# Kernel tuning notes

Hardware: AMD Instinct MI355X
Metric: run time of the kernel (lower is better)

## Reference

```python
import jax, jax.numpy as jnp
import numpy as np

B, T, C, H = 1, 1024, 2048, 32
N = C // H  # head_dim = 64
EPS_GN = 0.00064


def setup_inputs() -> dict:
    key = jax.random.key(0)
    ks = jax.random.split(key, 40)
    f32 = jnp.float32

    def rn(k, shape, s):
        return jax.random.normal(k, shape, f32) * s

    layer_idx, n_layer = 12, 24
    r01 = layer_idx / (n_layer - 1)
    r1a0 = 1.0 - layer_idx / n_layer
    ddd = (jnp.arange(C, dtype=f32) / C).reshape(1, 1, C)
    decay_speed = -7.0 + 5.0 * (jnp.arange(C, dtype=f32) / (C - 1)) ** (0.85 + r01 ** 0.5)

    inp = dict(
        hidden_states=jax.random.normal(ks[0], (B, T, C), f32),
        Wq=rn(ks[1], (C, C), 0.02), Wk=rn(ks[2], (C, C), 0.02),
        Wv=rn(ks[3], (C, C), 0.02), Wo=rn(ks[4], (C, C), 0.02),
        time_maa_x=1.0 - ddd ** (0.6 * r1a0 ** 0.9),
        time_maa_rg=rn(ks[5], (1, 1, C), 0.01),
        time_maa_wa=rn(ks[6], (1, 1, C), 0.01),
        time_maa_k=rn(ks[7], (1, 1, C), 0.01),
        time_maa_v=rn(ks[8], (1, 1, C), 0.01),
        time_maa_w1=rn(ks[9], (C, 4 * 32), 0.01),
        time_maa_w2=rn(ks[10], (4, 32, C), 0.01),
        time_decay=decay_speed.reshape(1, 1, C) + 0.5,
        time_decay_w1=rn(ks[11], (C, 64), 0.01),
        time_decay_w2=rn(ks[12], (64, C), 0.01),
        time_aaaaa=rn(ks[13], (1, 1, C), 0.01),
        time_aaa_w1=rn(ks[14], (C, 16), 0.01),
        time_aaa_w2=rn(ks[15], (16, C), 0.01),
        time_kkk_w1=rn(ks[16], (C, 16), 0.01),
        time_kkk_w2=rn(ks[17], (16, C), 0.01),
        gate_w1=rn(ks[18], (C, 128), 0.01),
        gate_w2=rn(ks[19], (128, C), 0.01),
        time_misc_a=rn(ks[20], (1, 1, C), 0.01),
        ma_w1=rn(ks[21], (C, 16), 0.01),
        ma_w2=rn(ks[22], (16, C), 0.01),
        time_misc_k=rn(ks[23], (1, 1, C), 0.01),
        mk_w1=rn(ks[24], (C, 16), 0.01),
        mk_w2=rn(ks[25], (16, C), 0.01),
        time_faaaa=rn(ks[26], (1, 1, H, N), 0.01),
        ln_w=1.0 + rn(ks[27], (C,), 0.01),
        ln_b=rn(ks[28], (C,), 0.01),
    )
    return inp


def _wkv7(r, w, k, v, a, b):
    """RWKV7 matrix-state recurrence. Inputs [B,T,C]; per head state [N,N].
    state_t = state * exp(w_t) (per key-col) + (state @ a_t) b_t^T + v_t k_t^T;
    out_t = state_t @ r_t."""
    hs = lambda x: x.reshape(B, T, H, N)
    r, k, v, a, b = map(hs, (r, k, v, a, b))
    dec = jnp.exp(hs(w))  # w <= -0.5, decay in (0,1)

    def step(state, inp):
        r_t, d_t, k_t, v_t, a_t, b_t = inp  # each [B,H,N]
        sa = jnp.einsum('bhij,bhj->bhi', state, a_t)
        state = (state * d_t[:, :, None, :]
                 + sa[..., None] * b_t[:, :, None, :]
                 + v_t[..., None] * k_t[:, :, None, :])
        out = jnp.einsum('bhij,bhj->bhi', state, r_t)
        return state, out

    xs = tuple(jnp.moveaxis(t, 1, 0) for t in (r, dec, k, v, a, b))  # [T,B,H,N]
    state0 = jnp.zeros((B, H, N, N), r.dtype)
    _, out = jax.lax.scan(step, state0, xs)
    return jnp.moveaxis(out, 0, 1).reshape(B, T, C)


def _group_norm(x, w, b):
    xg = x.reshape(B, T, H, N)
    mu = xg.mean(-1, keepdims=True)
    var = xg.var(-1, keepdims=True)
    xn = (xg - mu) * jax.lax.rsqrt(var + EPS_GN)
    return xn.reshape(B, T, C) * w + b


def reference(hidden_states, Wq, Wk, Wv, Wo, time_maa_x, time_maa_rg, time_maa_wa,
              time_maa_k, time_maa_v, time_maa_w1, time_maa_w2, time_decay,
              time_decay_w1, time_decay_w2, time_aaaaa, time_aaa_w1, time_aaa_w2,
              time_kkk_w1, time_kkk_w2, gate_w1, gate_w2, time_misc_a, ma_w1, ma_w2,
              time_misc_k, mk_w1, mk_w2, time_faaaa, ln_w, ln_b):
    x = hidden_states  # T already multiple of 16, so no padding branch
    dxprev = jnp.pad(x, ((0, 0), (1, 0), (0, 0)))[:, :-1] - x  # token shift
    xxx = x + dxprev * time_maa_x
    mix = jnp.tanh(xxx @ time_maa_w1).reshape(B, T, 4, 32)
    mix = jnp.einsum('btfd,fdc->fbtc', mix, time_maa_w2)  # [4,B,T,C]
    mrg, mwa, mk_mix, mv = mix[0], mix[1], mix[2], mix[3]
    xrg = x + dxprev * (time_maa_rg + mrg)
    xwa = x + dxprev * (time_maa_wa + mwa)
    xk = x + dxprev * (time_maa_k + mk_mix)
    xv = x + dxprev * (time_maa_v + mv)

    r = xrg @ Wq
    w = -jax.nn.softplus(-(time_decay + jnp.tanh(xwa @ time_decay_w1) @ time_decay_w2)) - 0.5
    k = xk @ Wk
    v = xv @ Wv
    g = jnp.tanh(xrg @ gate_w1) @ gate_w2

    kk = k + jnp.tanh(xk @ time_kkk_w1) @ time_kkk_w2
    kkh = kk.reshape(B, T, H, N)
    kk = (kkh / jnp.maximum(jnp.linalg.norm(kkh, axis=-1, keepdims=True), 1e-12)).reshape(B, T, C)

    a = jax.nn.sigmoid(time_aaaaa + (xwa @ time_aaa_w1) @ time_aaa_w2)
    ma = jax.nn.sigmoid(time_misc_a + (xwa @ ma_w1) @ ma_w2)
    k = k * ma + k * a * (1.0 - ma)
    mk_g = jax.nn.sigmoid(time_misc_k + (xk @ mk_w1) @ mk_w2)
    k = k * jnp.exp(jnp.minimum(w * mk_g, 0.0))

    y = _wkv7(r, w, k, v, -kk, kk * a)
    y = _group_norm(y, ln_w, ln_b)
    rh, kh, vh = (t.reshape(B, T, H, N) for t in (r, k, v))
    y = y + ((rh * kh * time_faaaa).sum(-1, keepdims=True) * vh).reshape(B, T, C)
    return (y * g) @ Wo
```

## Files before the change

kernel.cpp:

```cpp
#include <hip/hip_runtime.h>


#define T_ 1024
#define C_ 2048
#define H_ 32
#define N_ 64

using half8  = __attribute__((ext_vector_type(8))) _Float16;
using half4  = __attribute__((ext_vector_type(4))) _Float16;
using floatx4 = __attribute__((ext_vector_type(4))) float;

#define DPP_ADD(v, ctrl) \
    ((v) + __int_as_float(__builtin_amdgcn_update_dpp( \
        0, __float_as_int(v), (ctrl), 0xf, 0xf, true)))
#define REDUCE16(v) do { \
    v = DPP_ADD(v, 0xB1); v = DPP_ADD(v, 0x4E); \
    v = DPP_ADD(v, 0x141); v = DPP_ADD(v, 0x140); } while (0)

__device__ __forceinline__ void async_cp16(const void* g, void* l) {
    __builtin_amdgcn_global_load_lds(
        (const __attribute__((address_space(1))) void*)g,
        (__attribute__((address_space(3))) void*)l, 16, 0, 0);
}

__global__ __launch_bounds__(256) void k_tr(
    const float* __restrict__ W0, const float* __restrict__ W1,
    const float* __restrict__ W2, const float* __restrict__ W3,
    _Float16* __restrict__ D0, _Float16* __restrict__ D1,
    _Float16* __restrict__ D2, _Float16* __restrict__ D3)
{
    const int z = blockIdx.z;
    const float* S = (z == 0) ? W0 : (z == 1) ? W1 : (z == 2) ? W2 : W3;
    _Float16* D = (z == 0) ? D0 : (z == 1) ? D1 : (z == 2) ? D2 : D3;
    const int nb = blockIdx.x * 64, kb = blockIdx.y * 64;
    __shared__ __align__(16) float tile[64][65];
    const int tr = threadIdx.x >> 4, tc4 = (threadIdx.x & 15) * 4;
#pragma unroll
    for (int p = 0; p < 4; ++p) {
        int row = p * 16 + tr;
        float4 v = *(const float4*)&S[(size_t)(kb + row) * C_ + nb + tc4];
        tile[row][tc4 + 0] = v.x; tile[row][tc4 + 1] = v.y;
        tile[row][tc4 + 2] = v.z; tile[row][tc4 + 3] = v.w;
    }
    __syncthreads();
#pragma unroll
    for (int p = 0; p < 4; ++p) {
        int n = p * 16 + tr;
        half4 u;
        u[0] = (_Float16)tile[tc4 + 0][n];
        u[1] = (_Float16)tile[tc4 + 1][n];
        u[2] = (_Float16)tile[tc4 + 2][n];
        u[3] = (_Float16)tile[tc4 + 3][n];
        *(half4*)&D[(size_t)(nb + n) * C_ + kb + tc4] = u;
    }
}

__global__ __launch_bounds__(256) void k_trW(
    const float* __restrict__ maa_w1, const float* __restrict__ gate_w1,
    const float* __restrict__ decay_w1, const float* __restrict__ aaa_w1,
    const float* __restrict__ ma_w1, const float* __restrict__ kkk_w1,
    const float* __restrict__ mk_w1,
    _Float16* __restrict__ WTm, _Float16* __restrict__ WTl)
{
    const int z = blockIdx.z;
    const int k = blockIdx.x * 256 + threadIdx.x;
    const int n = blockIdx.y;
    if (z == 0 && n >= 128) return;
    const float* src; int stride, col;
    _Float16* dst;
    if (z == 0) { src = maa_w1; stride = 128; col = n; dst = WTm; }
    else {
        dst = WTl;
        if (n < 128)      { src = gate_w1;  stride = 128; col = n; }
        else if (n < 192) { src = decay_w1; stride = 64;  col = n - 128; }
        else if (n < 208) { src = aaa_w1;   stride = 16;  col = n - 192; }
        else if (n < 224) { src = ma_w1;    stride = 16;  col = n - 208; }
        else if (n < 240) { src = kkk_w1;   stride = 16;  col = n - 224; }
        else              { src = mk_w1;    stride = 16;  col = n - 240; }
    }
    dst[(size_t)n * C_ + k] = (_Float16)src[(size_t)k * stride + col];
}

__global__ __launch_bounds__(256) void k_prep(
    const float* __restrict__ X, const float* __restrict__ maa_x,
    _Float16* __restrict__ xxxH)
{
    const size_t idx = (size_t)blockIdx.x * 256 + threadIdx.x;
    const int c = (int)(idx & (C_ - 1));
    float cur = X[idx];
    float prev = (idx >= C_) ? X[idx - C_] : 0.0f;
    xxxH[idx] = (_Float16)(cur + (prev - cur) * maa_x[c]);
}

__global__ __launch_bounds__(256) void k_lora(
    int which,
    const _Float16* __restrict__ Axxx, const _Float16* __restrict__ Axrg,
    const _Float16* __restrict__ Axwa, const _Float16* __restrict__ Axk,
    const _Float16* __restrict__ WTm, const _Float16* __restrict__ WTl,
    float* __restrict__ m1p, float* __restrict__ l2p)
{
    const int mt = blockIdx.x;
    const int nt = blockIdx.y;
    const int ks = blockIdx.z;
    const _Float16* A; const _Float16* BT; float* O; int ostride;
    if (which == 0) { A = Axxx; BT = WTm; O = m1p; ostride = 128; }
    else {
        BT = WTl; O = l2p; ostride = 256;
        A = (nt < 4) ? Axrg : (nt < 7) ? Axwa : Axk;
    }
    O += (size_t)ks * T_ * ostride;
    const int m0 = mt * 64, n0 = nt * 32, k0 = ks * 512;
    const int tid = threadIdx.x;
    __shared__ __align__(16) _Float16 As[64 * 40];
    __shared__ __align__(16) _Float16 Bs[32 * 40];
    const int lane = tid & 63, wv = tid >> 6;
    const int r16 = lane & 15, q = lane >> 4;

    floatx4 acc[2];
    { floatx4 zv = {0.f, 0.f, 0.f, 0.f}; acc[0] = zv; acc[1] = zv; }

    const int arow = tid >> 2, ac8 = (tid & 3) * 8;
    const _Float16* ag = A + (size_t)(m0 + arow) * C_ + k0 + ac8;
    const _Float16* bg = BT + (size_t)(n0 + (tid >> 2)) * C_ + k0 + ac8;

    for (int kc = 0; kc < 512; kc += 32) {
        half8 av = *(const half8*)(ag + kc);
        half8 bv;
        if (tid < 128) bv = *(const half8*)(bg + kc);
        *(half8*)&As[arow * 40 + ac8] = av;
        if (tid < 128) *(half8*)&Bs[(tid >> 2) * 40 + ac8] = bv;
        __syncthreads();
        half8 af = *(const half8*)&As[(wv * 16 + r16) * 40 + q * 8];
        half8 b0 = *(const half8*)&Bs[(r16) * 40 + q * 8];
        half8 b1 = *(const half8*)&Bs[(16 + r16) * 40 + q * 8];
        acc[0] = __builtin_amdgcn_mfma_f32_16x16x32_f16(af, b0, acc[0], 0, 0, 0);
        acc[1] = __builtin_amdgcn_mfma_f32_16x16x32_f16(af, b1, acc[1], 0, 0, 0);
        __syncthreads();
    }
#pragma unroll
    for (int j = 0; j < 2; ++j)
#pragma unroll
        for (int e = 0; e < 4; ++e) {
            int row = m0 + wv * 16 + q * 4 + e;
            int col = n0 + j * 16 + r16;
            O[(size_t)row * ostride + col] = acc[j][e];
        }
}

__global__ __launch_bounds__(256) void k_xmix(
    const float* __restrict__ X, const float* __restrict__ m1p,
    const float* __restrict__ w2,
    const float* __restrict__ mrg, const float* __restrict__ mwa,
    const float* __restrict__ mk, const float* __restrict__ mv,
    _Float16* __restrict__ xrgH, _Float16* __restrict__ xwaH,
    _Float16* __restrict__ xkH, _Float16* __restrict__ xvH)
{
    const int tid = threadIdx.x;
    const int c = blockIdx.x * 256 + tid;
    const int t0 = blockIdx.y * 16;
    const size_t P = (size_t)T_ * 128;
    __shared__ __align__(16) float m1s[16][128];
#pragma unroll
    for (int p = 0; p < 2; ++p) {
        int id = tid + p * 256;
        int r = id >> 5, c4 = (id & 31) * 4;
        size_t off = (size_t)(t0 + r) * 128 + c4;
        float4 v0 = *(const float4*)&m1p[off];
        float4 v1 = *(const float4*)&m1p[P + off];
        float4 v2 = *(const float4*)&m1p[2 * P + off];
        float4 v3 = *(const float4*)&m1p[3 * P + off];
        float4 v;
        v.x = tanhf(((v0.x + v1.x) + v2.x) + v3.x);
        v.y = tanhf(((v0.y + v1.y) + v2.y) + v3.y);
        v.z = tanhf(((v0.z + v1.z) + v2.z) + v3.z);
        v.w = tanhf(((v0.w + v1.w) + v2.w) + v3.w);
        *(float4*)&m1s[r][c4] = v;
    }
    __syncthreads();
    float a0[16], a1[16], a2[16], a3[16];
#pragma unroll
    for (int t = 0; t < 16; ++t) { a0[t] = 0.f; a1[t] = 0.f; a2[t] = 0.f; a3[t] = 0.f; }
    for (int d = 0; d < 32; ++d) {
        float w0 = w2[(size_t)(0 * 32 + d) * C_ + c];
        float w1 = w2[(size_t)(1 * 32 + d) * C_ + c];
        float w2v = w2[(size_t)(2 * 32 + d) * C_ + c];
        float w3 = w2[(size_t)(3 * 32 + d) * C_ + c];
#pragma unroll
        for (int t = 0; t < 16; ++t) {
            a0[t] = fmaf(m1s[t][d],      w0,  a0[t]);
            a1[t] = fmaf(m1s[t][32 + d], w1,  a1[t]);
            a2[t] = fmaf(m1s[t][64 + d], w2v, a2[t]);
            a3[t] = fmaf(m1s[t][96 + d], w3,  a3[t]);
        }
    }
    float vrg = mrg[c], vwa = mwa[c], vmk = mk[c], vmv = mv[c];
    float prev = (t0 > 0) ? X[(size_t)(t0 - 1) * C_ + c] : 0.0f;
    for (int t = 0; t < 16; ++t) {
        size_t idx = (size_t)(t0 + t) * C_ + c;
        float cur = X[idx];
        float dx = prev - cur;
        xrgH[idx] = (_Float16)(cur + dx * (vrg + a0[t]));
        xwaH[idx] = (_Float16)(cur + dx * (vwa + a1[t]));
        xkH[idx]  = (_Float16)(cur + dx * (vmk + a2[t]));
        xvH[idx]  = (_Float16)(cur + dx * (vmv + a3[t]));
        prev = cur;
    }
}

__global__ __launch_bounds__(256) void k_gemm(
    const _Float16* __restrict__ A0, const _Float16* __restrict__ B0, float* __restrict__ C0,
    const _Float16* __restrict__ A1, const _Float16* __restrict__ B1, float* __restrict__ C1,
    const _Float16* __restrict__ A2, const _Float16* __restrict__ B2, float* __restrict__ C2)
{
    const int z = blockIdx.z;
    const _Float16* A = (z == 0) ? A0 : (z == 1) ? A1 : A2;
    const _Float16* Bt = (z == 0) ? B0 : (z == 1) ? B1 : B2;
    float* C = (z == 0) ? C0 : (z == 1) ? C1 : C2;
    const int mtile = blockIdx.y * 128;
    const int ntile = blockIdx.x * 128;
    const int tid = threadIdx.x;
    __shared__ __align__(16) _Float16 As[2][128 * 32];
    __shared__ __align__(16) _Float16 Bs[2][128 * 32];
    const int lane = tid & 63;
    const int wvid = tid >> 6;
    const int wm = wvid >> 1, wn = wvid & 1;
    const int r16 = lane & 15, q = lane >> 4;

    floatx4 acc[4][4];
#pragma unroll
    for (int i = 0; i < 4; ++i)
#pragma unroll
        for (int j = 0; j < 4; ++j) { floatx4 zv = {0.f, 0.f, 0.f, 0.f}; acc[i][j] = zv; }

    const int srow = tid >> 2, sq = tid & 3;
    const _Float16* agA = A + (size_t)(mtile + srow) * C_ + sq * 8;
    const _Float16* agB = Bt + (size_t)(ntile + srow) * C_ + sq * 8;
    const int ldso = srow * 32 + sq * 8;
    const size_t rowoff = (size_t)64 * C_;

    async_cp16(agA, &As[0][ldso]);
    async_cp16(agA + rowoff, &As[0][ldso + 64 * 32]);
    async_cp16(agB, &Bs[0][ldso]);
    async_cp16(agB + rowoff, &Bs[0][ldso + 64 * 32]);

    for (int kc = 0; kc < C_; kc += 32) {
        const int p = (kc >> 5) & 1;
        __syncthreads();
        if (kc + 32 < C_) {
            async_cp16(agA + kc + 32, &As[p ^ 1][ldso]);
            async_cp16(agA + kc + 32 + rowoff, &As[p ^ 1][ldso + 64 * 32]);
            async_cp16(agB + kc + 32, &Bs[p ^ 1][ldso]);
            async_cp16(agB + kc + 32 + rowoff, &Bs[p ^ 1][ldso + 64 * 32]);
        }
        half8 af[4], bf[4];
#pragma unroll
        for (int i = 0; i < 4; ++i)
            af[i] = *(const half8*)&As[p][(wm * 64 + i * 16 + r16) * 32 + q * 8];
#pragma unroll
        for (int j = 0; j < 4; ++j)
            bf[j] = *(const half8*)&Bs[p][(wn * 64 + j * 16 + r16) * 32 + q * 8];
#pragma unroll
        for (int i = 0; i < 4; ++i)
#pragma unroll
            for (int j = 0; j < 4; ++j)
                acc[i][j] = __builtin_amdgcn_mfma_f32_16x16x32_f16(af[i], bf[j], acc[i][j], 0, 0, 0);
    }
#pragma unroll
    for (int i = 0; i < 4; ++i)
#pragma unroll
        for (int j = 0; j < 4; ++j)
#pragma unroll
            for (int e = 0; e < 4; ++e) {
                int row = mtile + wm * 64 + i * 16 + q * 4 + e;
                int col = ntile + wn * 64 + j * 16 + r16;
                C[(size_t)row * C_ + col] = acc[i][j][e];
            }
}

__global__ __launch_bounds__(256) void k_fuse(
    const float* __restrict__ l2p,
    float* __restrict__ K0,
    const float* __restrict__ decay_w2, const float* __restrict__ aaa_w2,
    const float* __restrict__ ma_w2, const float* __restrict__ kkk_w2,
    const float* __restrict__ mk_w2,
    const float* __restrict__ tdecay, const float* __restrict__ aaaaa,
    const float* __restrict__ misc_a, const float* __restrict__ misc_k,
    float* __restrict__ Dout, float* __restrict__ KKout, float* __restrict__ Bout)
{
    const int tid = threadIdx.x;
    const int c = blockIdx.x * 256 + tid;
    const int t0 = blockIdx.y * 16;
    const size_t P = (size_t)T_ * 256;
    __shared__ __align__(16) float wsS[16][96];
    __shared__ __align__(16) float ksS[16][32];
    for (int id = tid; id < 16 * 24; id += 256) {
        int r = id / 24, c4 = (id % 24) * 4;
        size_t off = (size_t)(t0 + r) * 256 + 128 + c4;
        float4 v0 = *(const float4*)&l2p[off];
        float4 v1 = *(const float4*)&l2p[P + off];
        float4 v2 = *(const float4*)&l2p[2 * P + off];
        float4 v3 = *(const float4*)&l2p[3 * P + off];
        float4 v;
        v.x = ((v0.x + v1.x) + v2.x) + v3.x;
        v.y = ((v0.y + v1.y) + v2.y) + v3.y;
        v.z = ((v0.z + v1.z) + v2.z) + v3.z;
        v.w = ((v0.w + v1.w) + v2.w) + v3.w;
        if (c4 < 64) { v.x = tanhf(v.x); v.y = tanhf(v.y); v.z = tanhf(v.z); v.w = tanhf(v.w); }
        *(float4*)&wsS[r][c4] = v;
    }
    for (int id = tid; id < 16 * 8; id += 256) {
        int r = id / 8, c4 = (id % 8) * 4;
        size_t off = (size_t)(t0 + r) * 256 + 224 + c4;
        float4 v0 = *(const float4*)&l2p[off];
        float4 v1 = *(const float4*)&l2p[P + off];
        float4 v2 = *(const float4*)&l2p[2 * P + off];
        float4 v3 = *(const float4*)&l2p[3 * P + off];
        float4 v;
        v.x = ((v0.x + v1.x) + v2.x) + v3.x;
        v.y = ((v0.y + v1.y) + v2.y) + v3.y;
        v.z = ((v0.z + v1.z) + v2.z) + v3.z;
        v.w = ((v0.w + v1.w) + v2.w) + v3.w;
        if (c4 < 16) { v.x = tanhf(v.x); v.y = tanhf(v.y); v.z = tanhf(v.z); v.w = tanhf(v.w); }
        *(float4*)&ksS[r][c4] = v;
    }
    __syncthreads();
    float accW[16], accA[16], accMA[16], accKK[16], accMK[16];
#pragma unroll
    for (int r = 0; r < 16; ++r) { accW[r] = 0.f; accA[r] = 0.f; accMA[r] = 0.f; accKK[r] = 0.f; accMK[r] = 0.f; }
    for (int j = 0; j < 64; ++j) {
        float w = decay_w2[(size_t)j * C_ + c];
#pragma unroll
        for (int r = 0; r < 16; ++r) accW[r] = fmaf(wsS[r][j], w, accW[r]);
    }
    for (int j = 0; j < 16; ++j) {
        float wa = aaa_w2[(size_t)j * C_ + c];
        float wm = ma_w2[(size_t)j * C_ + c];
        float wk = kkk_w2[(size_t)j * C_ + c];
        float wq = mk_w2[(size_t)j * C_ + c];
#pragma unroll
        for (int r = 0; r < 16; ++r) {
            accA[r]  = fmaf(wsS[r][64 + j], wa, accA[r]);
            accMA[r] = fmaf(wsS[r][80 + j], wm, accMA[r]);
            accKK[r] = fmaf(ksS[r][j],      wk, accKK[r]);
            accMK[r] = fmaf(ksS[r][16 + j], wq, accMK[r]);
        }
    }
    float td = tdecay[c], aa = aaaaa[c], mia = misc_a[c], mik = misc_k[c];
    for (int r = 0; r < 16; ++r) {
        size_t idx = (size_t)(t0 + r) * C_ + c;
        float wraw = td + accW[r];
        float w = -logf(1.0f + __expf(-wraw)) - 0.5f;
        float a  = 1.0f / (1.0f + __expf(-(aa  + accA[r])));
        float mav = 1.0f / (1.0f + __expf(-(mia + accMA[r])));
        float mkv = 1.0f / (1.0f + __expf(-(mik + accMK[r])));
        float k0 = K0[idx];
        float kkun = k0 + accKK[r];
        float ss = kkun * kkun;
        REDUCE16(ss);
        ss += __shfl_xor(ss, 16, 64);
        ss += __shfl_xor(ss, 32, 64);
        float kn = kkun * (1.0f / fmaxf(sqrtf(ss), 1e-12f));
        Dout[idx]  = __expf(w);
        KKout[idx] = kn;
        Bout[idx]  = kn * a;
        K0[idx]    = k0 * (mav + a * (1.0f - mav)) * __expf(fminf(w * mkv, 0.0f));
    }
}

__global__ __launch_bounds__(1024) void k_wkv_p1(
    const float* __restrict__ DEC, const float* __restrict__ K,
    const float* __restrict__ V, const float* __restrict__ KK,
    const float* __restrict__ Bb,
    float* __restrict__ Send, float* __restrict__ Pend)
{
    const int tid = threadIdx.x;
    const int g = blockIdx.x;
    const int h = blockIdx.y;
    const bool isP = blockIdx.z != 0;
    const int c0 = h * 64;
    const int wv = tid >> 6, lane = tid & 63;
    const int row = wv * 4 + (lane >> 4);
    const int jg = lane & 15, j4 = jg * 4;

    __shared__ __align__(16) float dS[2][16][64], aS[2][16][64], bS[2][16][64],
                                   kS[2][16][64], vS[2][16][64];

    const int pos = tid & 255, grp = tid >> 8;
    const int pst = pos >> 4, pq4 = (pos & 15) * 4;

#define P1_STAGE(buf, tcb) do {                                               \
    size_t gg = (size_t)((tcb) + pst) * C_ + c0 + pq4;                        \
    if (grp == 0)      async_cp16(&DEC[gg], &dS[buf][pst][pq4]);              \
    else if (grp == 2) async_cp16(&KK[gg],  &aS[buf][pst][pq4]);              \
    else if (grp == 3) async_cp16(&Bb[gg],  &bS[buf][pst][pq4]);              \
    if (!isP) {                                                               \
        if (grp == 1)      async_cp16(&K[gg], &kS[buf][pst][pq4]);            \
        else if (grp == 0) async_cp16(&V[gg], &vS[buf][pst][pq4]);            \
    }                                                                         \
} while (0)

    float4 s;
    if (isP) {
        s.x = (j4 + 0 == row) ? 1.f : 0.f;
        s.y = (j4 + 1 == row) ? 1.f : 0.f;
        s.z = (j4 + 2 == row) ? 1.f : 0.f;
        s.w = (j4 + 3 == row) ? 1.f : 0.f;
    } else {
        s = make_float4(0.f, 0.f, 0.f, 0.f);
    }

    const int t0 = g * 128;
    P1_STAGE(0, t0);

    if (isP) {
        for (int tc = 0; tc < 128; tc += 16) {
            const int p = (tc >> 4) & 1;
            __syncthreads();
            if (tc + 16 < 128) P1_STAGE(p ^ 1, t0 + tc + 16);
#pragma unroll
            for (int tt = 0; tt < 16; ++tt) {
                float4 cd = *(float4*)&dS[p][tt][j4];
                float4 ca = *(float4*)&aS[p][tt][j4];
                float4 cb = *(float4*)&bS[p][tt][j4];
                float d01 = fmaf(s.y, ca.y, s.x * ca.x);
                float d23 = fmaf(s.w, ca.w, s.z * ca.z);
                float sa = -(d01 + d23);
                REDUCE16(sa);
                s.x = fmaf(s.x, cd.x, sa * cb.x);
                s.y = fmaf(s.y, cd.y, sa * cb.y);
                s.z = fmaf(s.z, cd.z, sa * cb.z);
                s.w = fmaf(s.w, cd.w, sa * cb.w);
            }
        }
        *(float4*)&Pend[(size_t)((h * 7 + g) * 64 + row) * 64 + j4] = s;
    } else {
        for (int tc = 0; tc < 128; tc += 16) {
            const int p = (tc >> 4) & 1;
            __syncthreads();
            if (tc + 16 < 128) P1_STAGE(p ^ 1, t0 + tc + 16);
#pragma unroll
            for (int tt = 0; tt < 16; ++tt) {
                float4 cd = *(float4*)&dS[p][tt][j4];
                float4 ca = *(float4*)&aS[p][tt][j4];
                float4 cb = *(float4*)&bS[p][tt][j4];
                float4 ck = *(float4*)&kS[p][tt][j4];
                float  cv = vS[p][tt][row];
                float d01 = fmaf(s.y, ca.y, s.x * ca.x);
                float d23 = fmaf(s.w, ca.w, s.z * ca.z);
                float sa = -(d01 + d23);
                REDUCE16(sa);
                s.x = fmaf(s.x, cd.x, fmaf(sa, cb.x, cv * ck.x));
                s.y = fmaf(s.y, cd.y, fmaf(sa, cb.y, cv * ck.y));
                s.z = fmaf(s.z, cd.z, fmaf(sa, cb.z, cv * ck.z));
                s.w = fmaf(s.w, cd.w, fmaf(sa, cb.w, cv * ck.w));
            }
        }
        *(float4*)&Send[(size_t)((h * 7 + g) * 64 + row) * 64 + j4] = s;
    }
#undef P1_STAGE
}

__global__ __launch_bounds__(256) void k_wkv_comb(
    const float* __restrict__ Send, const float* __restrict__ Pend,
    float* __restrict__ Sin)
{
    const int h = blockIdx.x;
    const int tid = threadIdx.x;
    const int i = tid >> 2;
    const int jq = (tid & 3) * 16;
    __shared__ float Sc[64][65];
    __shared__ __align__(16) float Pl[64][64];

    float4 z4 = make_float4(0.f, 0.f, 0.f, 0.f);
#pragma unroll
    for (int c = 0; c < 16; c += 4)
        *(float4*)&Sin[(size_t)(h * 8) * 4096 + (size_t)i * 64 + jq + c] = z4;
#pragma unroll
    for (int c = 0; c < 16; ++c) Sc[i][jq + c] = 0.f;
    __syncthreads();

    for (int g = 1; g < 8; ++g) {
        const float* Pg = &Pend[(size_t)(h * 7 + g - 1) * 4096];
        for (int idx = tid * 4; idx < 4096; idx += 1024) {
            float4 v = *(const float4*)&Pg[idx];
            *(float4*)&Pl[idx >> 6][idx & 63] = v;
        }
        __syncthreads();
        float acc[16];
        const float* Sg = &Send[(size_t)(h * 7 + g - 1) * 4096 + (size_t)i * 64 + jq];
#pragma unroll
        for (int c = 0; c < 16; c += 4) {
            float4 v = *(const float4*)&Sg[c];
            acc[c] = v.x; acc[c + 1] = v.y; acc[c + 2] = v.z; acc[c + 3] = v.w;
        }
        for (int k = 0; k < 64; ++k) {
            float sik = Sc[i][k];
#pragma unroll
            for (int c = 0; c < 16; ++c) acc[c] = fmaf(sik, Pl[k][jq + c], acc[c]);
        }
        __syncthreads();
        float* So = &Sin[(size_t)(h * 8 + g) * 4096 + (size_t)i * 64 + jq];
#pragma unroll
        for (int c = 0; c < 16; ++c) Sc[i][jq + c] = acc[c];
#pragma unroll
        for (int c = 0; c < 16; c += 4) {
            float4 v = make_float4(acc[c], acc[c + 1], acc[c + 2], acc[c + 3]);
            *(float4*)&So[c] = v;
        }
        __syncthreads();
    }
}

__global__ __launch_bounds__(1024) void k_wkv_p2(
    const float* __restrict__ R, const float* __restrict__ DEC,
    const float* __restrict__ K, const float* __restrict__ V,
    const float* __restrict__ KK, const float* __restrict__ Bb,
    const float* __restrict__ Sin, float* __restrict__ Y)
{
    const int tid = threadIdx.x;
    const int g = blockIdx.x;
    const int h = blockIdx.y;
    const int c0 = h * 64;
    const int wv = tid >> 6, lane = tid & 63;
    const int row = wv * 4 + (lane >> 4);
    const int jg = lane & 15, j4 = jg * 4;

    __shared__ __align__(16) float rS[2][16][64], dS[2][16][64], kS[2][16][64],
                                   aS[2][16][64], bS[2][16][64], vS[2][16][64];

    const int pos = tid & 255, grp = tid >> 8;
    const int pst = pos >> 4, pq4 = (pos & 15) * 4;

#define P2_STAGE(buf, tcb) do {                                               \
    size_t gg = (size_t)((tcb) + pst) * C_ + c0 + pq4;                        \
    if (grp == 0)      { async_cp16(&R[gg], &rS[buf][pst][pq4]);              \
                         async_cp16(&K[gg], &kS[buf][pst][pq4]); }            \
    else if (grp == 1) { async_cp16(&DEC[gg], &dS[buf][pst][pq4]);            \
                         async_cp16(&V[gg],   &vS[buf][pst][pq4]); }          \
    else if (grp == 2) async_cp16(&KK[gg], &aS[buf][pst][pq4]);               \
    else               async_cp16(&Bb[gg], &bS[buf][pst][pq4]);               \
} while (0)

    float4 s = *(const float4*)&Sin[(size_t)((h * 8 + g) * 64 + row) * 64 + j4];

    const int t0 = g * 128;
    P2_STAGE(0, t0);

    for (int tc = 0; tc < 128; tc += 16) {
        const int p = (tc >> 4) & 1;
        __syncthreads();
        if (tc + 16 < 128) P2_STAGE(p ^ 1, t0 + tc + 16);
#pragma unroll
        for (int hh = 0; hh < 2; ++hh) {
            float po[8];
#pragma unroll
            for (int q = 0; q < 8; ++q) {
                const int tt = hh * 8 + q;
                float4 cr = *(float4*)&rS[p][tt][j4];
                float4 cd = *(float4*)&dS[p][tt][j4];
                float4 ck = *(float4*)&kS[p][tt][j4];
                float4 ca = *(float4*)&aS[p][tt][j4];
                float4 cb = *(float4*)&bS[p][tt][j4];
                float  cv = vS[p][tt][row];
                float d01 = fmaf(s.y, ca.y, s.x * ca.x);
                float d23 = fmaf(s.w, ca.w, s.z * ca.z);
                float sa = -(d01 + d23);
                REDUCE16(sa);
                s.x = fmaf(s.x, cd.x, fmaf(sa, cb.x, cv * ck.x));
                s.y = fmaf(s.y, cd.y, fmaf(sa, cb.y, cv * ck.y));
                s.z = fmaf(s.z, cd.z, fmaf(sa, cb.z, cv * ck.z));
                s.w = fmaf(s.w, cd.w, fmaf(sa, cb.w, cv * ck.w));
                po[q] = fmaf(s.w, cr.w, fmaf(s.z, cr.z, fmaf(s.y, cr.y, s.x * cr.x)));
            }
#pragma unroll
            for (int q = 0; q < 8; ++q) REDUCE16(po[q]);
            if (jg == 0) {
#pragma unroll
                for (int q = 0; q < 8; ++q)
                    Y[(size_t)(t0 + tc + hh * 8 + q) * C_ + c0 + row] = po[q];
            }
        }
    }
#undef P2_STAGE
}

__global__ __launch_bounds__(256) void k_gn(
    const float* __restrict__ Y, const float* __restrict__ R, const float* __restrict__ K,
    const float* __restrict__ V, const float* __restrict__ l2p,
    const float* __restrict__ gw2,
    const float* __restrict__ faaaa, const float* __restrict__ lnw,
    const float* __restrict__ lnb, _Float16* __restrict__ YG)
{
    const int tid = threadIdx.x;
    const int c = blockIdx.x * 256 + tid;
    const int t0 = blockIdx.y * 16;
    const size_t P = (size_t)T_ * 256;
    __shared__ __align__(16) float gs[16][128];
    for (int id = tid; id < 16 * 128; id += 256) {
        int r = id >> 7, cc = id & 127;
        size_t off = (size_t)(t0 + r) * 256 + cc;
        float v = ((l2p[off] + l2p[P + off]) + l2p[2 * P + off]) + l2p[3 * P + off];
        gs[r][cc] = tanhf(v);
    }
    __syncthreads();
    float gacc[16];
#pragma unroll
    for (int r = 0; r < 16; ++r) gacc[r] = 0.f;
    for (int j = 0; j < 128; ++j) {
        float w = gw2[(size_t)j * C_ + c];
#pragma unroll
        for (int r = 0; r < 16; ++r) gacc[r] = fmaf(gs[r][j], w, gacc[r]);
    }
    float fa = faaaa[c], lw = lnw[c], lb = lnb[c];
    for (int r = 0; r < 16; ++r) {
        const size_t idx = (size_t)(t0 + r) * C_ + c;
        float y = Y[idx];
        float s1 = y, s2 = y * y;
#pragma unroll
        for (int off = 1; off < 64; off <<= 1) {
            s1 += __shfl_xor(s1, off, 64);
            s2 += __shfl_xor(s2, off, 64);
        }
        float mu = s1 * (1.0f / 64.0f);
        float var = s2 * (1.0f / 64.0f) - mu * mu;
        float gn = (y - mu) * rsqrtf(var + 0.00064f) * lw + lb;
        float p = R[idx] * K[idx] * fa;
#pragma unroll
        for (int off = 1; off < 64; off <<= 1) p += __shfl_xor(p, off, 64);
        float y2 = gn + p * V[idx];
        YG[idx] = (_Float16)(y2 * gacc[r]);
    }
}

extern "C" void kernel_launch(void* const* d_in, const int* in_sizes, int n_in,
                              void* d_out, int out_size, void* d_ws, size_t ws_size,
                              hipStream_t stream)
{
    (void)in_sizes; (void)n_in; (void)out_size; (void)ws_size;
    const float* hidden   = (const float*)d_in[0];
    const float* Wq       = (const float*)d_in[1];
    const float* Wk       = (const float*)d_in[2];
    const float* Wv       = (const float*)d_in[3];
    const float* Wo       = (const float*)d_in[4];
    const float* maa_x    = (const float*)d_in[5];
    const float* maa_rg   = (const float*)d_in[6];
    const float* maa_wa   = (const float*)d_in[7];
    const float* maa_k    = (const float*)d_in[8];
    const float* maa_v    = (const float*)d_in[9];
    const float* maa_w1   = (const float*)d_in[10];
    const float* maa_w2   = (const float*)d_in[11];
    const float* tdecay   = (const float*)d_in[12];
    const float* decay_w1 = (const float*)d_in[13];
    const float* decay_w2 = (const float*)d_in[14];
    const float* aaaaa    = (const float*)d_in[15];
    const float* aaa_w1   = (const float*)d_in[16];
    const float* aaa_w2   = (const float*)d_in[17];
    const float* kkk_w1   = (const float*)d_in[18];
    const float* kkk_w2   = (const float*)d_in[19];
    const float* gate_w1  = (const float*)d_in[20];
    const float* gate_w2  = (const float*)d_in[21];
    const float* misc_a   = (const float*)d_in[22];
    const float* ma_w1    = (const float*)d_in[23];
    const float* ma_w2    = (const float*)d_in[24];
    const float* misc_k   = (const float*)d_in[25];
    const float* mk_w1    = (const float*)d_in[26];
    const float* mk_w2    = (const float*)d_in[27];
    const float* faaaa    = (const float*)d_in[28];
    const float* lnw      = (const float*)d_in[29];
    const float* lnb      = (const float*)d_in[30];

    float* ws = (float*)d_ws;
    const size_t TC = (size_t)T_ * C_;
    float* S0 = ws + 0 * TC;
    float* Send = ws + 1 * TC;
    float* Pend = Send + (size_t)32 * 7 * 64 * 64;
    float* S2 = ws + 2 * TC;
    float* S3 = ws + 3 * TC;
    float* S4 = ws + 4 * TC;
    float* S5 = ws + 5 * TC;
    float* S6 = ws + 6 * TC;
    float* S7 = ws + 7 * TC;
    float* m1p = ws + 8 * TC;
    float* l2p = m1p + (size_t)4 * T_ * 128;
    _Float16* WTq = (_Float16*)(l2p + (size_t)4 * T_ * 256);
    _Float16* WTk = WTq + (size_t)C_ * C_;
    _Float16* WTv = WTk + (size_t)C_ * C_;
    _Float16* WTo = WTv + (size_t)C_ * C_;
    _Float16* WTm = WTo + (size_t)C_ * C_;
    _Float16* WTl = WTm + (size_t)128 * C_;
    _Float16* xxxH = WTl + (size_t)256 * C_;
    _Float16* xrgH = xxxH + TC;
    _Float16* xwaH = xrgH + TC;
    _Float16* xkH  = xwaH + TC;
    _Float16* xvH  = xkH + TC;
    _Float16* ygH  = xxxH;
    float* Sin = (float*)xrgH;
    float* out = (float*)d_out;

    k_tr<<<dim3(32, 32, 4), 256, 0, stream>>>(Wq, Wk, Wv, Wo, WTq, WTk, WTv, WTo);
    k_trW<<<dim3(8, 256, 2), 256, 0, stream>>>(maa_w1, gate_w1, decay_w1,
        aaa_w1, ma_w1, kkk_w1, mk_w1, WTm, WTl);
    k_prep<<<dim3((int)(TC / 256)), 256, 0, stream>>>(hidden, maa_x, xxxH);
    k_lora<<<dim3(16, 4, 4), 256, 0, stream>>>(0, xxxH, xxxH, xxxH, xxxH,
        WTm, WTl, m1p, l2p);
    k_xmix<<<dim3(8, 64), 256, 0, stream>>>(hidden, m1p, maa_w2,
        maa_rg, maa_wa, maa_k, maa_v, xrgH, xwaH, xkH, xvH);
    k_lora<<<dim3(16, 8, 4), 256, 0, stream>>>(1, xxxH, xrgH, xwaH, xkH,
        WTm, WTl, m1p, l2p);
    k_gemm<<<dim3(16, 8, 3), 256, 0, stream>>>(
        xrgH, WTq, S4,  xkH, WTk, S6,  xvH, WTv, S7);
    k_fuse<<<dim3(8, 64), 256, 0, stream>>>(l2p, S6, decay_w2, aaa_w2, ma_w2,
        kkk_w2, mk_w2, tdecay, aaaaa, misc_a, misc_k, S5, S3, S2);
    k_wkv_p1<<<dim3(7, 32, 2), 1024, 0, stream>>>(S5, S6, S7, S3, S2, Send, Pend);
    k_wkv_comb<<<dim3(32), 256, 0, stream>>>(Send, Pend, Sin);
    k_wkv_p2<<<dim3(8, 32), 1024, 0, stream>>>(S4, S5, S6, S7, S3, S2, Sin, S0);
    k_gn<<<dim3(8, 64), 256, 0, stream>>>(S0, S4, S6, S7, l2p, gate_w2,
        faaaa, lnw, lnb, ygH);
    k_gemm<<<dim3(16, 8, 1), 256, 0, stream>>>(
        ygH, WTo, out,  ygH, WTo, out,  ygH, WTo, out);
}
```

Before: 558.1 us.

## Give each WKV lane four state rows and shrink k_fuse time tiles

The WKV scan kernels now assign four state rows per lane instead of one. p2 shrinks from 1024 to 256 threads and p1 merges its S and P variants into one 512-thread block, so the shared-memory reads of decay/a/b/k are reused across four rows and fewer lanes run the recurrence. k_fuse now processes 4 timesteps per block instead of 16, launching four times more blocks, and uses the fast __logf. Trade-offs are more register pressure per lane, fewer waves to hide latency, and slightly lower precision in the log.

```diff
diff --git a/kernel.cpp b/kernel.cpp
--- a/kernel.cpp
+++ b/kernel.cpp
@@ -289,12 +289,12 @@
 {
     const int tid = threadIdx.x;
     const int c = blockIdx.x * 256 + tid;
-    const int t0 = blockIdx.y * 16;
+    const int t0 = blockIdx.y * 4;
     const size_t P = (size_t)T_ * 256;
-    __shared__ __align__(16) float wsS[16][96];
-    __shared__ __align__(16) float ksS[16][32];
-    for (int id = tid; id < 16 * 24; id += 256) {
-        int r = id / 24, c4 = (id % 24) * 4;
+    __shared__ __align__(16) float wsS[4][96];
+    __shared__ __align__(16) float ksS[4][32];
+    if (tid < 4 * 24) {
+        int r = tid / 24, c4 = (tid % 24) * 4;
         size_t off = (size_t)(t0 + r) * 256 + 128 + c4;
         float4 v0 = *(const float4*)&l2p[off];
         float4 v1 = *(const float4*)&l2p[P + off];
@@ -308,8 +308,8 @@
         if (c4 < 64) { v.x = tanhf(v.x); v.y = tanhf(v.y); v.z = tanhf(v.z); v.w = tanhf(v.w); }
         *(float4*)&wsS[r][c4] = v;
     }
-    for (int id = tid; id < 16 * 8; id += 256) {
-        int r = id / 8, c4 = (id % 8) * 4;
+    if (tid < 4 * 8) {
+        int r = tid / 8, c4 = (tid % 8) * 4;
         size_t off = (size_t)(t0 + r) * 256 + 224 + c4;
         float4 v0 = *(const float4*)&l2p[off];
         float4 v1 = *(const float4*)&l2p[P + off];
@@ -324,13 +324,13 @@
         *(float4*)&ksS[r][c4] = v;
     }
     __syncthreads();
-    float accW[16], accA[16], accMA[16], accKK[16], accMK[16];
-#pragma unroll
-    for (int r = 0; r < 16; ++r) { accW[r] = 0.f; accA[r] = 0.f; accMA[r] = 0.f; accKK[r] = 0.f; accMK[r] = 0.f; }
+    float accW[4], accA[4], accMA[4], accKK[4], accMK[4];
+#pragma unroll
+    for (int r = 0; r < 4; ++r) { accW[r] = 0.f; accA[r] = 0.f; accMA[r] = 0.f; accKK[r] = 0.f; accMK[r] = 0.f; }
     for (int j = 0; j < 64; ++j) {
         float w = decay_w2[(size_t)j * C_ + c];
 #pragma unroll
-        for (int r = 0; r < 16; ++r) accW[r] = fmaf(wsS[r][j], w, accW[r]);
+        for (int r = 0; r < 4; ++r) accW[r] = fmaf(wsS[r][j], w, accW[r]);
     }
     for (int j = 0; j < 16; ++j) {
         float wa = aaa_w2[(size_t)j * C_ + c];
@@ -338,7 +338,7 @@
         float wk = kkk_w2[(size_t)j * C_ + c];
         float wq = mk_w2[(size_t)j * C_ + c];
 #pragma unroll
-        for (int r = 0; r < 16; ++r) {
+        for (int r = 0; r < 4; ++r) {
             accA[r]  = fmaf(wsS[r][64 + j], wa, accA[r]);
             accMA[r] = fmaf(wsS[r][80 + j], wm, accMA[r]);
             accKK[r] = fmaf(ksS[r][j],      wk, accKK[r]);
@@ -346,10 +346,11 @@
         }
     }
     float td = tdecay[c], aa = aaaaa[c], mia = misc_a[c], mik = misc_k[c];
-    for (int r = 0; r < 16; ++r) {
+#pragma unroll
+    for (int r = 0; r < 4; ++r) {
         size_t idx = (size_t)(t0 + r) * C_ + c;
         float wraw = td + accW[r];
-        float w = -logf(1.0f + __expf(-wraw)) - 0.5f;
+        float w = -__logf(1.0f + __expf(-wraw)) - 0.5f;
         float a  = 1.0f / (1.0f + __expf(-(aa  + accA[r])));
         float mav = 1.0f / (1.0f + __expf(-(mia + accMA[r])));
         float mkv = 1.0f / (1.0f + __expf(-(mik + accMK[r])));
@@ -367,7 +368,7 @@
     }
 }
 
-__global__ __launch_bounds__(1024) void k_wkv_p1(
+__global__ __launch_bounds__(512) void k_wkv_p1(
     const float* __restrict__ DEC, const float* __restrict__ K,
     const float* __restrict__ V, const float* __restrict__ KK,
     const float* __restrict__ Bb,
@@ -376,87 +377,88 @@
     const int tid = threadIdx.x;
     const int g = blockIdx.x;
     const int h = blockIdx.y;
-    const bool isP = blockIdx.z != 0;
     const int c0 = h * 64;
     const int wv = tid >> 6, lane = tid & 63;
-    const int row = wv * 4 + (lane >> 4);
-    const int jg = lane & 15, j4 = jg * 4;
-
-    __shared__ __align__(16) float dS[2][16][64], aS[2][16][64], bS[2][16][64],
-                                   kS[2][16][64], vS[2][16][64];
+    const int jg = lane & 15, q = lane >> 4, j4 = jg * 4;
+    const bool isS = wv < 4;
+    const int row0 = (isS ? wv : wv - 4) * 16 + q * 4;
+
+    __shared__ __align__(16) float dS[2][16][64], kS[2][16][64], vS[2][16][64],
+                                   aS[2][16][64], bS[2][16][64];
 
     const int pos = tid & 255, grp = tid >> 8;
     const int pst = pos >> 4, pq4 = (pos & 15) * 4;
 
 #define P1_STAGE(buf, tcb) do {                                               \
     size_t gg = (size_t)((tcb) + pst) * C_ + c0 + pq4;                        \
-    if (grp == 0)      async_cp16(&DEC[gg], &dS[buf][pst][pq4]);              \
-    else if (grp == 2) async_cp16(&KK[gg],  &aS[buf][pst][pq4]);              \
-    else if (grp == 3) async_cp16(&Bb[gg],  &bS[buf][pst][pq4]);              \
-    if (!isP) {                                                               \
-        if (grp == 1)      async_cp16(&K[gg], &kS[buf][pst][pq4]);            \
-        else if (grp == 0) async_cp16(&V[gg], &vS[buf][pst][pq4]);            \
-    }                                                                         \
+    if (grp == 0) { async_cp16(&DEC[gg], &dS[buf][pst][pq4]);                 \
+                    async_cp16(&KK[gg],  &aS[buf][pst][pq4]);                 \
+                    async_cp16(&Bb[gg],  &bS[buf][pst][pq4]); }               \
+    else          { async_cp16(&K[gg], &kS[buf][pst][pq4]);                   \
+                    async_cp16(&V[gg], &vS[buf][pst][pq4]); }                 \
 } while (0)
 
-    float4 s;
-    if (isP) {
-        s.x = (j4 + 0 == row) ? 1.f : 0.f;
-        s.y = (j4 + 1 == row) ? 1.f : 0.f;
-        s.z = (j4 + 2 == row) ? 1.f : 0.f;
-        s.w = (j4 + 3 == row) ? 1.f : 0.f;
+    float4 s0, s1, s2, s3;
+    if (isS) {
+        s0 = make_float4(0.f, 0.f, 0.f, 0.f); s1 = s0; s2 = s0; s3 = s0;
     } else {
-        s = make_float4(0.f, 0.f, 0.f, 0.f);
+#define IDROW(m) make_float4((j4 + 0 == row0 + (m)) ? 1.f : 0.f,              \
+                             (j4 + 1 == row0 + (m)) ? 1.f : 0.f,              \
+                             (j4 + 2 == row0 + (m)) ? 1.f : 0.f,              \
+                             (j4 + 3 == row0 + (m)) ? 1.f : 0.f)
+        s0 = IDROW(0); s1 = IDROW(1); s2 = IDROW(2); s3 = IDROW(3);
+#undef IDROW
     }
 
     const int t0 = g * 128;
     P1_STAGE(0, t0);
 
-    if (isP) {
-        for (int tc = 0; tc < 128; tc += 16) {
-            const int p = (tc >> 4) & 1;
-            __syncthreads();
-            if (tc + 16 < 128) P1_STAGE(p ^ 1, t0 + tc + 16);
-#pragma unroll
-            for (int tt = 0; tt < 16; ++tt) {
-                float4 cd = *(float4*)&dS[p][tt][j4];
-                float4 ca = *(float4*)&aS[p][tt][j4];
-                float4 cb = *(float4*)&bS[p][tt][j4];
-                float d01 = fmaf(s.y, ca.y, s.x * ca.x);
-                float d23 = fmaf(s.w, ca.w, s.z * ca.z);
-                float sa = -(d01 + d23);
-                REDUCE16(sa);
-                s.x = fmaf(s.x, cd.x, sa * cb.x);
-                s.y = fmaf(s.y, cd.y, sa * cb.y);
-                s.z = fmaf(s.z, cd.z, sa * cb.z);
-                s.w = fmaf(s.w, cd.w, sa * cb.w);
+    for (int tc = 0; tc < 128; tc += 16) {
+        const int p = (tc >> 4) & 1;
+        __syncthreads();
+        if (tc + 16 < 128) P1_STAGE(p ^ 1, t0 + tc + 16);
+#pragma unroll
+        for (int tt = 0; tt < 16; ++tt) {
+            float4 cd = *(float4*)&dS[p][tt][j4];
+            float4 ca = *(float4*)&aS[p][tt][j4];
+            float4 cb = *(float4*)&bS[p][tt][j4];
+            float4 ck, vv;
+            if (isS) {
+                ck = *(float4*)&kS[p][tt][j4];
+                vv = *(float4*)&vS[p][tt][row0];
+            } else {
+                ck = make_float4(0.f, 0.f, 0.f, 0.f);
+                vv = make_float4(0.f, 0.f, 0.f, 0.f);
             }
-        }
-        *(float4*)&Pend[(size_t)((h * 7 + g) * 64 + row) * 64 + j4] = s;
-    } else {
-        for (int tc = 0; tc < 128; tc += 16) {
-            const int p = (tc >> 4) & 1;
-            __syncthreads();
-            if (tc + 16 < 128) P1_STAGE(p ^ 1, t0 + tc + 16);
-#pragma unroll
-            for (int tt = 0; tt < 16; ++tt) {
-                float4 cd = *(float4*)&dS[p][tt][j4];
-                float4 ca = *(float4*)&aS[p][tt][j4];
-                float4 cb = *(float4*)&bS[p][tt][j4];
-                float4 ck = *(float4*)&kS[p][tt][j4];
-                float  cv = vS[p][tt][row];
-                float d01 = fmaf(s.y, ca.y, s.x * ca.x);
-                float d23 = fmaf(s.w, ca.w, s.z * ca.z);
-                float sa = -(d01 + d23);
-                REDUCE16(sa);
-                s.x = fmaf(s.x, cd.x, fmaf(sa, cb.x, cv * ck.x));
-                s.y = fmaf(s.y, cd.y, fmaf(sa, cb.y, cv * ck.y));
-                s.z = fmaf(s.z, cd.z, fmaf(sa, cb.z, cv * ck.z));
-                s.w = fmaf(s.w, cd.w, fmaf(sa, cb.w, cv * ck.w));
-            }
-        }
-        *(float4*)&Send[(size_t)((h * 7 + g) * 64 + row) * 64 + j4] = s;
-    }
+            float sa0 = -(fmaf(s0.y, ca.y, s0.x * ca.x) + fmaf(s0.w, ca.w, s0.z * ca.z));
+            float sa1 = -(fmaf(s1.y, ca.y, s1.x * ca.x) + fmaf(s1.w, ca.w, s1.z * ca.z));
+            float sa2 = -(fmaf(s2.y, ca.y, s2.x * ca.x) + fmaf(s2.w, ca.w, s2.z * ca.z));
+            float sa3 = -(fmaf(s3.y, ca.y, s3.x * ca.x) + fmaf(s3.w, ca.w, s3.z * ca.z));
+            REDUCE16(sa0); REDUCE16(sa1); REDUCE16(sa2); REDUCE16(sa3);
+            s0.x = fmaf(s0.x, cd.x, fmaf(sa0, cb.x, vv.x * ck.x));
+            s0.y = fmaf(s0.y, cd.y, fmaf(sa0, cb.y, vv.x * ck.y));
+            s0.z = fmaf(s0.z, cd.z, fmaf(sa0, cb.z, vv.x * ck.z));
+            s0.w = fmaf(s0.w, cd.w, fmaf(sa0, cb.w, vv.x * ck.w));
+            s1.x = fmaf(s1.x, cd.x, fmaf(sa1, cb.x, vv.y * ck.x));
+            s1.y = fmaf(s1.y, cd.y, fmaf(sa1, cb.y, vv.y * ck.y));
+            s1.z = fmaf(s1.z, cd.z, fmaf(sa1, cb.z, vv.y * ck.z));
+            s1.w = fmaf(s1.w, cd.w, fmaf(sa1, cb.w, vv.y * ck.w));
+            s2.x = fmaf(s2.x, cd.x, fmaf(sa2, cb.x, vv.z * ck.x));
+            s2.y = fmaf(s2.y, cd.y, fmaf(sa2, cb.y, vv.z * ck.y));
+            s2.z = fmaf(s2.z, cd.z, fmaf(sa2, cb.z, vv.z * ck.z));
+            s2.w = fmaf(s2.w, cd.w, fmaf(sa2, cb.w, vv.z * ck.w));
+            s3.x = fmaf(s3.x, cd.x, fmaf(sa3, cb.x, vv.w * ck.x));
+            s3.y = fmaf(s3.y, cd.y, fmaf(sa3, cb.y, vv.w * ck.y));
+            s3.z = fmaf(s3.z, cd.z, fmaf(sa3, cb.z, vv.w * ck.z));
+            s3.w = fmaf(s3.w, cd.w, fmaf(sa3, cb.w, vv.w * ck.w));
+        }
+    }
+    float* dst = isS ? Send : Pend;
+    size_t base = (size_t)((h * 7 + g) * 64 + row0) * 64 + j4;
+    *(float4*)&dst[base +   0] = s0;
+    *(float4*)&dst[base +  64] = s1;
+    *(float4*)&dst[base + 128] = s2;
+    *(float4*)&dst[base + 192] = s3;
 #undef P1_STAGE
 }
 
@@ -511,7 +513,7 @@
     }
 }
 
-__global__ __launch_bounds__(1024) void k_wkv_p2(
+__global__ __launch_bounds__(256) void k_wkv_p2(
     const float* __restrict__ R, const float* __restrict__ DEC,
     const float* __restrict__ K, const float* __restrict__ V,
     const float* __restrict__ KK, const float* __restrict__ Bb,
@@ -522,26 +524,32 @@
     const int h = blockIdx.y;
     const int c0 = h * 64;
     const int wv = tid >> 6, lane = tid & 63;
-    const int row = wv * 4 + (lane >> 4);
-    const int jg = lane & 15, j4 = jg * 4;
+    const int jg = lane & 15, q = lane >> 4, j4 = jg * 4;
+    const int row0 = wv * 16 + q * 4;
 
     __shared__ __align__(16) float rS[2][16][64], dS[2][16][64], kS[2][16][64],
                                    aS[2][16][64], bS[2][16][64], vS[2][16][64];
 
-    const int pos = tid & 255, grp = tid >> 8;
-    const int pst = pos >> 4, pq4 = (pos & 15) * 4;
+    const int pst = tid >> 4, pq4 = (tid & 15) * 4;
 
 #define P2_STAGE(buf, tcb) do {                                               \
     size_t gg = (size_t)((tcb) + pst) * C_ + c0 + pq4;                        \
-    if (grp == 0)      { async_cp16(&R[gg], &rS[buf][pst][pq4]);              \
-                         async_cp16(&K[gg], &kS[buf][pst][pq4]); }            \
-    else if (grp == 1) { async_cp16(&DEC[gg], &dS[buf][pst][pq4]);            \
-                         async_cp16(&V[gg],   &vS[buf][pst][pq4]); }          \
-    else if (grp == 2) async_cp16(&KK[gg], &aS[buf][pst][pq4]);               \
-    else               async_cp16(&Bb[gg], &bS[buf][pst][pq4]);               \
+    async_cp16(&R[gg],   &rS[buf][pst][pq4]);                                 \
+    async_cp16(&DEC[gg], &dS[buf][pst][pq4]);                                 \
+    async_cp16(&K[gg],   &kS[buf][pst][pq4]);                                 \
+    async_cp16(&V[gg],   &vS[buf][pst][pq4]);                                 \
+    async_cp16(&KK[gg],  &aS[buf][pst][pq4]);                                 \
+    async_cp16(&Bb[gg],  &bS[buf][pst][pq4]);                                 \
 } while (0)
 
-    float4 s = *(const float4*)&Sin[(size_t)((h * 8 + g) * 64 + row) * 64 + j4];
+    float4 s0, s1, s2, s3;
+    {
+        const float* Sb = &Sin[(size_t)((h * 8 + g) * 64 + row0) * 64 + j4];
+        s0 = *(const float4*)&Sb[0];
+        s1 = *(const float4*)&Sb[64];
+        s2 = *(const float4*)&Sb[128];
+        s3 = *(const float4*)&Sb[192];
+    }
 
     const int t0 = g * 128;
     P2_STAGE(0, t0);
@@ -552,32 +560,53 @@
         if (tc + 16 < 128) P2_STAGE(p ^ 1, t0 + tc + 16);
 #pragma unroll
         for (int hh = 0; hh < 2; ++hh) {
-            float po[8];
-#pragma unroll
-            for (int q = 0; q < 8; ++q) {
-                const int tt = hh * 8 + q;
+            float po0[8], po1[8], po2[8], po3[8];
+#pragma unroll
+            for (int qs = 0; qs < 8; ++qs) {
+                const int tt = hh * 8 + qs;
                 float4 cr = *(float4*)&rS[p][tt][j4];
                 float4 cd = *(float4*)&dS[p][tt][j4];
                 float4 ck = *(float4*)&kS[p][tt][j4];
                 float4 ca = *(float4*)&aS[p][tt][j4];
                 float4 cb = *(float4*)&bS[p][tt][j4];
-                float  cv = vS[p][tt][row];
-                float d01 = fmaf(s.y, ca.y, s.x * ca.x);
-                float d23 = fmaf(s.w, ca.w, s.z * ca.z);
-                float sa = -(d01 + d23);
-                REDUCE16(sa);
-                s.x = fmaf(s.x, cd.x, fmaf(sa, cb.x, cv * ck.x));
-                s.y = fmaf(s.y, cd.y, fmaf(sa, cb.y, cv * ck.y));
-                s.z = fmaf(s.z, cd.z, fmaf(sa, cb.z, cv * ck.z));
-                s.w = fmaf(s.w, cd.w, fmaf(sa, cb.w, cv * ck.w));
-                po[q] = fmaf(s.w, cr.w, fmaf(s.z, cr.z, fmaf(s.y, cr.y, s.x * cr.x)));
+                float4 vv = *(float4*)&vS[p][tt][row0];
+                float sa0 = -(fmaf(s0.y, ca.y, s0.x * ca.x) + fmaf(s0.w, ca.w, s0.z * ca.z));
+                float sa1 = -(fmaf(s1.y, ca.y, s1.x * ca.x) + fmaf(s1.w, ca.w, s1.z * ca.z));
+                float sa2 = -(fmaf(s2.y, ca.y, s2.x * ca.x) + fmaf(s2.w, ca.w, s2.z * ca.z));
+                float sa3 = -(fmaf(s3.y, ca.y, s3.x * ca.x) + fmaf(s3.w, ca.w, s3.z * ca.z));
+                REDUCE16(sa0); REDUCE16(sa1); REDUCE16(sa2); REDUCE16(sa3);
+                s0.x = fmaf(s0.x, cd.x, fmaf(sa0, cb.x, vv.x * ck.x));
+                s0.y = fmaf(s0.y, cd.y, fmaf(sa0, cb.y, vv.x * ck.y));
+                s0.z = fmaf(s0.z, cd.z, fmaf(sa0, cb.z, vv.x * ck.z));
+                s0.w = fmaf(s0.w, cd.w, fmaf(sa0, cb.w, vv.x * ck.w));
+                s1.x = fmaf(s1.x, cd.x, fmaf(sa1, cb.x, vv.y * ck.x));
+                s1.y = fmaf(s1.y, cd.y, fmaf(sa1, cb.y, vv.y * ck.y));
+                s1.z = fmaf(s1.z, cd.z, fmaf(sa1, cb.z, vv.y * ck.z));
+                s1.w = fmaf(s1.w, cd.w, fmaf(sa1, cb.w, vv.y * ck.w));
+                s2.x = fmaf(s2.x, cd.x, fmaf(sa2, cb.x, vv.z * ck.x));
+                s2.y = fmaf(s2.y, cd.y, fmaf(sa2, cb.y, vv.z * ck.y));
+                s2.z = fmaf(s2.z, cd.z, fmaf(sa2, cb.z, vv.z * ck.z));
+                s2.w = fmaf(s2.w, cd.w, fmaf(sa2, cb.w, vv.z * ck.w));
+                s3.x = fmaf(s3.x, cd.x, fmaf(sa3, cb.x, vv.w * ck.x));
+                s3.y = fmaf(s3.y, cd.y, fmaf(sa3, cb.y, vv.w * ck.y));
+                s3.z = fmaf(s3.z, cd.z, fmaf(sa3, cb.z, vv.w * ck.z));
+                s3.w = fmaf(s3.w, cd.w, fmaf(sa3, cb.w, vv.w * ck.w));
+                po0[qs] = fmaf(s0.w, cr.w, fmaf(s0.z, cr.z, fmaf(s0.y, cr.y, s0.x * cr.x)));
+                po1[qs] = fmaf(s1.w, cr.w, fmaf(s1.z, cr.z, fmaf(s1.y, cr.y, s1.x * cr.x)));
+                po2[qs] = fmaf(s2.w, cr.w, fmaf(s2.z, cr.z, fmaf(s2.y, cr.y, s2.x * cr.x)));
+                po3[qs] = fmaf(s3.w, cr.w, fmaf(s3.z, cr.z, fmaf(s3.y, cr.y, s3.x * cr.x)));
             }
 #pragma unroll
-            for (int q = 0; q < 8; ++q) REDUCE16(po[q]);
+            for (int qs = 0; qs < 8; ++qs) {
+                REDUCE16(po0[qs]); REDUCE16(po1[qs]);
+                REDUCE16(po2[qs]); REDUCE16(po3[qs]);
+            }
             if (jg == 0) {
 #pragma unroll
-                for (int q = 0; q < 8; ++q)
-                    Y[(size_t)(t0 + tc + hh * 8 + q) * C_ + c0 + row] = po[q];
+                for (int qs = 0; qs < 8; ++qs) {
+                    float4 o = make_float4(po0[qs], po1[qs], po2[qs], po3[qs]);
+                    *(float4*)&Y[(size_t)(t0 + tc + hh * 8 + qs) * C_ + c0 + row0] = o;
+                }
             }
         }
     }
@@ -709,11 +738,11 @@
         WTm, WTl, m1p, l2p);
     k_gemm<<<dim3(16, 8, 3), 256, 0, stream>>>(
         xrgH, WTq, S4,  xkH, WTk, S6,  xvH, WTv, S7);
-    k_fuse<<<dim3(8, 64), 256, 0, stream>>>(l2p, S6, decay_w2, aaa_w2, ma_w2,
+    k_fuse<<<dim3(8, 256), 256, 0, stream>>>(l2p, S6, decay_w2, aaa_w2, ma_w2,
         kkk_w2, mk_w2, tdecay, aaaaa, misc_a, misc_k, S5, S3, S2);
-    k_wkv_p1<<<dim3(7, 32, 2), 1024, 0, stream>>>(S5, S6, S7, S3, S2, Send, Pend);
+    k_wkv_p1<<<dim3(7, 32), 512, 0, stream>>>(S5, S6, S7, S3, S2, Send, Pend);
     k_wkv_comb<<<dim3(32), 256, 0, stream>>>(Send, Pend, Sin);
-    k_wkv_p2<<<dim3(8, 32), 1024, 0, stream>>>(S4, S5, S6, S7, S3, S2, Sin, S0);
+    k_wkv_p2<<<dim3(8, 32), 256, 0, stream>>>(S4, S5, S6, S7, S3, S2, Sin, S0);
     k_gn<<<dim3(8, 64), 256, 0, stream>>>(S0, S4, S6, S7, l2p, gate_w2,
         faaaa, lnw, lnb, ygH);
     k_gemm<<<dim3(16, 8, 1), 256, 0, stream>>>(
```

Measured after the change: 524.4 us. 6.0% less time.
